# Optimization experiments

Measured on AMD Instinct MI355X. Metric: run time of the kernel, lower is better.

The kernel has to match this reference:

```python
import jax, jax.numpy as jnp
import numpy as np

VOCAB = 100000
EMBED = 128
CONTEXT = 2  # context_size
B, L = 64, 2048


def setup_inputs() -> dict:
    key = jax.random.key(0)
    k1, k2 = jax.random.split(key)
    x = jax.random.randint(k1, (B, L), 0, VOCAB, dtype=jnp.int64)
    emb = jax.random.normal(k2, (VOCAB, EMBED), dtype=jnp.float32)
    return {"x": x, "emb": emb}


def reference(x, emb):
    # x: [B, L] int token ids; emb: [V, E]
    Bn, Ln = x.shape
    C = CONTEXT
    j = jnp.arange(Ln)  # positions
    # ordering matches torch: before = x[j-1], x[j-2], ..., x[j-C]; after = x[j+1..j+C]
    offsets = jnp.concatenate([-jnp.arange(1, C + 1), jnp.arange(1, C + 1)])  # [2C]
    idx = j[:, None] + offsets[None, :]  # [L, 2C]
    valid = (idx >= 0) & (idx < Ln)
    idx_c = jnp.clip(idx, 0, Ln - 1)
    tok = jnp.where(valid[None, :, :], x[:, idx_c], 0)  # [B, L, 2C]; OOB -> token 0
    # embedding gather then sum over the sequence dim (dim=1 in torch code)
    out = jnp.sum(emb[tok], axis=1)  # [B, 2C, E]
    return out
```

## Files before the change

kernel.cpp:

```cpp
#include <hip/hip_runtime.h>

#define EMBED  128
#define BATCH  64
#define SEQLEN 2048
#define NSLICE 4
#define SLICEF 32
#define BLOCK  1024
#define NROWG  (BLOCK / 8)
#define TOKPG  (SEQLEN / NROWG)

__device__ __forceinline__ float4 f4add(const float4 a, const float4 b) {
    return make_float4(a.x + b.x, a.y + b.y, a.z + b.z, a.w + b.w);
}
__device__ __forceinline__ float4 f4sub(const float4 a, const float4 b) {
    return make_float4(a.x - b.x, a.y - b.y, a.z - b.z, a.w - b.w);
}
__device__ __forceinline__ float4 f4shfl_xor(const float4 v, int mask) {
    return make_float4(__shfl_xor(v.x, mask), __shfl_xor(v.y, mask),
                       __shfl_xor(v.z, mask), __shfl_xor(v.w, mask));
}

__global__ __launch_bounds__(BLOCK) void cbow_onepass_kernel(
    const int* __restrict__ x, const float* __restrict__ emb,
    float* __restrict__ out) {
    const int idx = blockIdx.x;
    const int sl  = (idx & 7) >> 1;
    const int b   = ((idx >> 3) << 1) | (idx & 1);
    const int tid = threadIdx.x;
    const int c   = tid & 7;
    const int r   = tid >> 3;
    const int w   = tid >> 6;
    const int ln  = tid & 63;

    const float* embs = emb + sl * SLICEF + c * 4;

    float4 e0v, v0v, v1v, vl2v, vl1v;
    if (tid < 32) {
        const int ec  = tid & 7;
        const float* embe = emb + sl * SLICEF + ec * 4;
        const int t0  = x[b * SEQLEN + 0];
        const int t1  = x[b * SEQLEN + 1];
        const int tl2 = x[b * SEQLEN + SEQLEN - 2];
        const int tl1 = x[b * SEQLEN + SEQLEN - 1];
        e0v  = *reinterpret_cast<const float4*>(embe);
        v0v  = *reinterpret_cast<const float4*>(embe + (size_t)t0  * EMBED);
        v1v  = *reinterpret_cast<const float4*>(embe + (size_t)t1  * EMBED);
        vl2v = *reinterpret_cast<const float4*>(embe + (size_t)tl2 * EMBED);
        vl1v = *reinterpret_cast<const float4*>(embe + (size_t)tl1 * EMBED);
    }

    __shared__ int    toks[SEQLEN];
    __shared__ float4 psum[16][8];

    reinterpret_cast<int2*>(toks)[tid] =
        reinterpret_cast<const int2*>(x + b * SEQLEN)[tid];
    __syncthreads();

    float4 a0 = make_float4(0.f, 0.f, 0.f, 0.f);
    float4 a1 = a0, a2 = a0, a3 = a0;
#pragma unroll
    for (int it = 0; it < TOKPG; it += 4) {
        const float4 v0 = *reinterpret_cast<const float4*>(
            embs + (size_t)toks[r + NROWG * (it + 0)] * EMBED);
        const float4 v1 = *reinterpret_cast<const float4*>(
            embs + (size_t)toks[r + NROWG * (it + 1)] * EMBED);
        const float4 v2 = *reinterpret_cast<const float4*>(
            embs + (size_t)toks[r + NROWG * (it + 2)] * EMBED);
        const float4 v3 = *reinterpret_cast<const float4*>(
            embs + (size_t)toks[r + NROWG * (it + 3)] * EMBED);
        a0 = f4add(a0, v0);
        a1 = f4add(a1, v1);
        a2 = f4add(a2, v2);
        a3 = f4add(a3, v3);
    }
    float4 acc = f4add(f4add(a0, a1), f4add(a2, a3));

    acc = f4add(acc, f4shfl_xor(acc, 8));
    acc = f4add(acc, f4shfl_xor(acc, 16));
    acc = f4add(acc, f4shfl_xor(acc, 32));
    if (ln < 8) psum[w][c] = acc;
    __syncthreads();

    if (w == 0) {
        const int g = ln >> 3;
        float4 t = f4add(psum[g][c], psum[g + 8][c]);
        t = f4add(t, f4shfl_xor(t, 8));
        t = f4add(t, f4shfl_xor(t, 16));
        t = f4add(t, f4shfl_xor(t, 32));
        if (ln < 8) psum[0][c] = t;
    }
    __syncthreads();

    if (tid < 32) {
        const int o = tid >> 3;
        const float4 S = psum[0][c];
        float4 res = f4add(S, e0v);
        if (o == 0) {
            res = f4sub(res, vl1v);
        } else if (o == 1) {
            res = f4add(f4sub(f4sub(res, vl1v), vl2v), e0v);
        } else if (o == 2) {
            res = f4sub(res, v0v);
        } else {
            res = f4add(f4sub(f4sub(res, v0v), v1v), e0v);
        }
        *reinterpret_cast<float4*>(
            out + ((size_t)b * 4 + o) * EMBED + sl * SLICEF + c * 4) = res;
    }
}

extern "C" void kernel_launch(void* const* d_in, const int* in_sizes, int n_in,
                              void* d_out, int out_size, void* d_ws, size_t ws_size,
                              hipStream_t stream) {
    const int*   x   = (const int*)d_in[0];
    const float* emb = (const float*)d_in[1];
    float*       out = (float*)d_out;

    cbow_onepass_kernel<<<dim3(BATCH * NSLICE), dim3(BLOCK), 0, stream>>>(
        x, emb, out);
}
```

Baseline: 14.21 us.

## Halve block size, load tokens directly into registers, drop LDS staging and a barrier

Shrinks blocks from 1024 to 512 threads, so each thread now handles 32 tokens instead of 16. Each thread loads its token ids straight from global memory into registers instead of staging the whole sequence in shared memory behind a barrier. It then issues 32 independent embedding gathers into 8 accumulators, which exposes more memory-level parallelism per thread. The final reduction and output write are folded into wave 0, removing one __syncthreads; the trade-off is fewer resident threads and higher register pressure.

```diff
diff --git a/kernel.cpp b/kernel.cpp
--- a/kernel.cpp
+++ b/kernel.cpp
@@ -5,7 +5,7 @@
 #define SEQLEN 2048
 #define NSLICE 4
 #define SLICEF 32
-#define BLOCK  1024
+#define BLOCK  512
 #define NROWG  (BLOCK / 8)
 #define TOKPG  (SEQLEN / NROWG)
 
@@ -32,80 +32,71 @@
     const int w   = tid >> 6;
     const int ln  = tid & 63;
 
+    const int*   xb   = x + b * SEQLEN;
     const float* embs = emb + sl * SLICEF + c * 4;
 
     float4 e0v, v0v, v1v, vl2v, vl1v;
     if (tid < 32) {
-        const int ec  = tid & 7;
-        const float* embe = emb + sl * SLICEF + ec * 4;
-        const int t0  = x[b * SEQLEN + 0];
-        const int t1  = x[b * SEQLEN + 1];
-        const int tl2 = x[b * SEQLEN + SEQLEN - 2];
-        const int tl1 = x[b * SEQLEN + SEQLEN - 1];
-        e0v  = *reinterpret_cast<const float4*>(embe);
-        v0v  = *reinterpret_cast<const float4*>(embe + (size_t)t0  * EMBED);
-        v1v  = *reinterpret_cast<const float4*>(embe + (size_t)t1  * EMBED);
-        vl2v = *reinterpret_cast<const float4*>(embe + (size_t)tl2 * EMBED);
-        vl1v = *reinterpret_cast<const float4*>(embe + (size_t)tl1 * EMBED);
+        const int t0  = xb[0];
+        const int t1  = xb[1];
+        const int tl2 = xb[SEQLEN - 2];
+        const int tl1 = xb[SEQLEN - 1];
+        e0v  = *reinterpret_cast<const float4*>(embs);
+        v0v  = *reinterpret_cast<const float4*>(embs + (size_t)t0  * EMBED);
+        v1v  = *reinterpret_cast<const float4*>(embs + (size_t)t1  * EMBED);
+        vl2v = *reinterpret_cast<const float4*>(embs + (size_t)tl2 * EMBED);
+        vl1v = *reinterpret_cast<const float4*>(embs + (size_t)tl1 * EMBED);
     }
 
-    __shared__ int    toks[SEQLEN];
-    __shared__ float4 psum[16][8];
+    int tk[TOKPG];
+#pragma unroll
+    for (int it = 0; it < TOKPG; ++it) tk[it] = xb[r + NROWG * it];
 
-    reinterpret_cast<int2*>(toks)[tid] =
-        reinterpret_cast<const int2*>(x + b * SEQLEN)[tid];
-    __syncthreads();
+    float4 acc[8];
+#pragma unroll
+    for (int i = 0; i < 8; ++i) acc[i] = make_float4(0.f, 0.f, 0.f, 0.f);
+#pragma unroll
+    for (int it = 0; it < TOKPG; ++it) {
+        const float4 v = *reinterpret_cast<const float4*>(
+            embs + (size_t)tk[it] * EMBED);
+        acc[it & 7] = f4add(acc[it & 7], v);
+    }
+    float4 s01 = f4add(acc[0], acc[1]);
+    float4 s23 = f4add(acc[2], acc[3]);
+    float4 s45 = f4add(acc[4], acc[5]);
+    float4 s67 = f4add(acc[6], acc[7]);
+    float4 a = f4add(f4add(s01, s23), f4add(s45, s67));
 
-    float4 a0 = make_float4(0.f, 0.f, 0.f, 0.f);
-    float4 a1 = a0, a2 = a0, a3 = a0;
-#pragma unroll
-    for (int it = 0; it < TOKPG; it += 4) {
-        const float4 v0 = *reinterpret_cast<const float4*>(
-            embs + (size_t)toks[r + NROWG * (it + 0)] * EMBED);
-        const float4 v1 = *reinterpret_cast<const float4*>(
-            embs + (size_t)toks[r + NROWG * (it + 1)] * EMBED);
-        const float4 v2 = *reinterpret_cast<const float4*>(
-            embs + (size_t)toks[r + NROWG * (it + 2)] * EMBED);
-        const float4 v3 = *reinterpret_cast<const float4*>(
-            embs + (size_t)toks[r + NROWG * (it + 3)] * EMBED);
-        a0 = f4add(a0, v0);
-        a1 = f4add(a1, v1);
-        a2 = f4add(a2, v2);
-        a3 = f4add(a3, v3);
-    }
-    float4 acc = f4add(f4add(a0, a1), f4add(a2, a3));
+    a = f4add(a, f4shfl_xor(a, 8));
+    a = f4add(a, f4shfl_xor(a, 16));
+    a = f4add(a, f4shfl_xor(a, 32));
 
-    acc = f4add(acc, f4shfl_xor(acc, 8));
-    acc = f4add(acc, f4shfl_xor(acc, 16));
-    acc = f4add(acc, f4shfl_xor(acc, 32));
-    if (ln < 8) psum[w][c] = acc;
+    __shared__ float4 psum[8][8];
+    if (ln < 8) psum[w][c] = a;
     __syncthreads();
 
     if (w == 0) {
         const int g = ln >> 3;
-        float4 t = f4add(psum[g][c], psum[g + 8][c]);
+        float4 t = psum[g & 7][c];
         t = f4add(t, f4shfl_xor(t, 8));
         t = f4add(t, f4shfl_xor(t, 16));
         t = f4add(t, f4shfl_xor(t, 32));
-        if (ln < 8) psum[0][c] = t;
-    }
-    __syncthreads();
 
-    if (tid < 32) {
-        const int o = tid >> 3;
-        const float4 S = psum[0][c];
-        float4 res = f4add(S, e0v);
-        if (o == 0) {
-            res = f4sub(res, vl1v);
-        } else if (o == 1) {
-            res = f4add(f4sub(f4sub(res, vl1v), vl2v), e0v);
-        } else if (o == 2) {
-            res = f4sub(res, v0v);
-        } else {
-            res = f4add(f4sub(f4sub(res, v0v), v1v), e0v);
+        if (ln < 32) {
+            const int o = ln >> 3;
+            float4 res = f4add(t, e0v);
+            if (o == 0) {
+                res = f4sub(res, vl1v);
+            } else if (o == 1) {
+                res = f4add(f4sub(f4sub(res, vl1v), vl2v), e0v);
+            } else if (o == 2) {
+                res = f4sub(res, v0v);
+            } else {
+                res = f4add(f4sub(f4sub(res, v0v), v1v), e0v);
+            }
+            *reinterpret_cast<float4*>(
+                out + ((size_t)b * 4 + o) * EMBED + sl * SLICEF + c * 4) = res;
         }
-        *reinterpret_cast<float4*>(
-            out + ((size_t)b * 4 + o) * EMBED + sl * SLICEF + c * 4) = res;
     }
 }
 
```

Measured after the change: 15.10 us (median of 2 runs). +6.2%, slower.
